# Kernel optimization log

Hardware: AMD Instinct MI355X
Metric: run time of the kernel (lower is better)

Reference implementation:

```python
import jax, jax.numpy as jnp
import numpy as np

BETA = 0.01  # soft-threshold level (init kwarg)
EPS = 1e-12


def vector_to_toeplitz(v):
    # v: [2N-1] complex generator; T[i, j] = v[N-1 + i - j], shape [N, N]
    n = (v.shape[0] + 1) // 2
    ii = jnp.arange(n)[:, None]
    jj = jnp.arange(n)[None, :]
    return v[(n - 1) + ii - jj]


def soft_thresh(z, beta):
    # complex soft-threshold (proximal op of beta*||.||_1):
    # z * max(|z| - beta, 0) / |z|
    mag = jnp.abs(z)
    scale = jnp.maximum(mag - beta, 0.0) / jnp.maximum(mag, EPS)
    return z * scale.astype(z.real.dtype)


def setup_inputs() -> dict:
    key = jax.random.key(0)
    ks = jax.random.split(key, 8)
    N, M, B = 1024, 256, 1024
    d = jnp.float32
    return {
        "v_re": jax.random.normal(ks[0], (2 * N - 1,), d),
        "v_im": jax.random.normal(ks[1], (2 * N - 1,), d),
        "W2_re": jax.random.normal(ks[2], (N, M), d) / np.sqrt(M),
        "W2_im": jax.random.normal(ks[3], (N, M), d) / np.sqrt(M),
        "x_re": jax.random.normal(ks[4], (N, B), d),
        "x_im": jax.random.normal(ks[5], (N, B), d),
        "y_re": jax.random.normal(ks[6], (M, B), d),
        "y_im": jax.random.normal(ks[7], (M, B), d),
    }


def reference(v_re, v_im, W2_re, W2_im, x_re, x_im, y_re, y_im):
    v = jax.lax.complex(v_re, v_im)      # [2N-1]
    W2 = jax.lax.complex(W2_re, W2_im)   # [N, M] (= A^H)
    x = jax.lax.complex(x_re, x_im)      # [N, B]
    y = jax.lax.complex(y_re, y_im)      # [M, B]
    W1 = vector_to_toeplitz(v)           # [N, N] Toeplitz
    # tpm(W1, x) + W2 @ y, then complex soft-threshold
    z = soft_thresh(W1 @ x + W2 @ y, BETA)  # [N, B]
    return z
```

## Files before the change

kernel.cpp:

```cpp
#include <hip/hip_runtime.h>
#include <hip/hip_fp16.h>
#include <cstdint>
#include <cstddef>


#define K_DIM 2560
#define BETA_F 0.01f
#define EPS_F  1e-12f

typedef __attribute__((ext_vector_type(8))) _Float16 half8;
typedef __attribute__((ext_vector_type(4))) _Float16 half4;
typedef __attribute__((ext_vector_type(4))) float   floatx4;

__device__ alignas(16) _Float16 g_Ap[1024 * K_DIM];
__device__ alignas(16) _Float16 g_Bt[2048 * K_DIM];

__global__ __launch_bounds__(256) void build_all(
    const float* __restrict__ v_re, const float* __restrict__ v_im,
    const float* __restrict__ W2_re, const float* __restrict__ W2_im,
    const float* __restrict__ x_re, const float* __restrict__ x_im,
    const float* __restrict__ y_re, const float* __restrict__ y_im)
{
    const int bx = blockIdx.x;
    if (bx < 1280) {
        int t = bx * 256 + threadIdx.x;
        int i  = t / 320;
        int c  = t - i * 320;
        int kp = c * 8;
        half8 h;
        if (kp < 1024) {
#pragma unroll
            for (int j = 0; j < 8; ++j) h[j] = (_Float16)v_re[1023 + i - kp - j];
        } else if (kp < 1280) {
            const float* s = W2_re + i * 256 + (kp - 1024);
#pragma unroll
            for (int j = 0; j < 8; ++j) h[j] = (_Float16)s[j];
        } else if (kp < 2304) {
            int k2 = kp - 1280;
#pragma unroll
            for (int j = 0; j < 8; ++j) h[j] = (_Float16)v_im[1023 + i - k2 - j];
        } else {
            const float* s = W2_im + i * 256 + (kp - 2304);
#pragma unroll
            for (int j = 0; j < 8; ++j) h[j] = (_Float16)s[j];
        }
        *reinterpret_cast<half8*>(g_Ap + (size_t)i * K_DIM + kp) = h;
        return;
    }
    __shared__ float lre[32][33];
    __shared__ float lim[32][33];
    int idx = bx - 1280;
    int bk  = idx % 40;
    int by  = idx / 40;
    const float* sre = (bk < 32) ? x_re : y_re;
    const float* sim = (bk < 32) ? x_im : y_im;
    int kb   = (bk < 32) ? bk : (bk - 32);
    int koff = (bk < 32) ? 0 : 1024;
    int k0 = kb * 32;
    int n0 = by * 32;
    int tid = threadIdx.x;
    int tx = tid & 31, ty = tid >> 5;
#pragma unroll
    for (int s = 0; s < 4; ++s) {
        int kk = ty + 8 * s;
        lre[kk][tx] = sre[(size_t)(k0 + kk) * 1024 + n0 + tx];
        lim[kk][tx] = sim[(size_t)(k0 + kk) * 1024 + n0 + tx];
    }
    __syncthreads();
    int lane_n = tid >> 3;
    int kq     = (tid & 7) * 4;
    half4 hre, him, hmim;
#pragma unroll
    for (int j = 0; j < 4; ++j) {
        float re = lre[kq + j][lane_n];
        float im = lim[kq + j][lane_n];
        hre[j]  = (_Float16)re;
        him[j]  = (_Float16)im;
        hmim[j] = (_Float16)(-im);
    }
    int n = n0 + lane_n;
    size_t kk2 = (size_t)koff + k0 + kq;
    _Float16* r0 = g_Bt + (size_t)(2 * n)     * K_DIM;
    _Float16* r1 = g_Bt + (size_t)(2 * n + 1) * K_DIM;
    *reinterpret_cast<half4*>(r0 + kk2)        = hre;
    *reinterpret_cast<half4*>(r0 + kk2 + 1280) = hmim;
    *reinterpret_cast<half4*>(r1 + kk2)        = him;
    *reinterpret_cast<half4*>(r1 + kk2 + 1280) = hre;
}

__global__ __launch_bounds__(256, 4) void gemm_fused(float* __restrict__ out,
                                                     int out_n)
{
    __shared__ __align__(16) _Float16 As[2 * 2 * 64 * 32];
    __shared__ __align__(16) _Float16 Bs[2 * 2 * 64 * 32];

    const int tid  = threadIdx.x;
    const int lane = tid & 63;
    const int w    = tid >> 6;
    const int wm   = w >> 1;
    const int wn   = w & 1;

    const int bid = blockIdx.x;
    const int xcd = bid & 7;
    const int t   = bid >> 3;
    const int mi0 = ((xcd & 1) * 8 + (t & 7)) * 64;
    const int ni0 = ((xcd >> 1) * 8 + (t >> 3)) * 64;

    floatx4 acc[2][2];
#pragma unroll
    for (int a = 0; a < 2; ++a)
#pragma unroll
        for (int b = 0; b < 2; ++b) acc[a][b] = (floatx4)0.0f;

    const int rS = tid >> 2;
    const int jS = tid & 3;
    const int s0 = ((rS & 15) >> 1) & 3;
    char* asW = (char*)As + rS * 64 + ((jS ^ s0) * 16);
    char* bsW = (char*)Bs + rS * 64 + ((jS ^ s0) * 16);
    const _Float16* gA = g_Ap + (size_t)(mi0 + rS) * K_DIM + jS * 8;
    const _Float16* gB = g_Bt + (size_t)(ni0 + rS) * K_DIM + jS * 8;

    const int rowA = lane & 15;
    const int q    = lane >> 4;
    const int coff = (q ^ ((rowA >> 1) & 3)) * 16;

    const int NIT = K_DIM / 64;

    half8 sA0[2], sA1[2], sB0[2], sB1[2];

    {
        half8 a0 = *reinterpret_cast<const half8*>(gA);
        half8 a1 = *reinterpret_cast<const half8*>(gA + 32);
        half8 b0 = *reinterpret_cast<const half8*>(gB);
        half8 b1 = *reinterpret_cast<const half8*>(gB + 32);
        sA0[1] = *reinterpret_cast<const half8*>(gA + 64);
        sA1[1] = *reinterpret_cast<const half8*>(gA + 96);
        sB0[1] = *reinterpret_cast<const half8*>(gB + 64);
        sB1[1] = *reinterpret_cast<const half8*>(gB + 96);
        *reinterpret_cast<half8*>(asW)        = a0;
        *reinterpret_cast<half8*>(asW + 4096) = a1;
        *reinterpret_cast<half8*>(bsW)        = b0;
        *reinterpret_cast<half8*>(bsW + 4096) = b1;
    }
    __syncthreads();

#pragma unroll 2
    for (int kt = 0; kt < NIT; ++kt) {
        const int cur = kt & 1;
        const int nxt = cur ^ 1;
        if (kt + 2 < NIT) {
            const _Float16* ga = gA + (size_t)(kt + 2) * 64;
            const _Float16* gb = gB + (size_t)(kt + 2) * 64;
            sA0[cur] = *reinterpret_cast<const half8*>(ga);
            sA1[cur] = *reinterpret_cast<const half8*>(ga + 32);
            sB0[cur] = *reinterpret_cast<const half8*>(gb);
            sB1[cur] = *reinterpret_cast<const half8*>(gb + 32);
        }
        const char* Ab = (const char*)As + cur * 8192;
        const char* Bb = (const char*)Bs + cur * 8192;
        half8 af[2][2], bf[2][2];
#pragma unroll
        for (int mi = 0; mi < 2; ++mi) {
            int r = wm * 32 + mi * 16 + rowA;
            af[mi][0] = *reinterpret_cast<const half8*>(Ab + r * 64 + coff);
            af[mi][1] = *reinterpret_cast<const half8*>(Ab + 4096 + r * 64 + coff);
        }
#pragma unroll
        for (int ni = 0; ni < 2; ++ni) {
            int r = wn * 32 + ni * 16 + rowA;
            bf[ni][0] = *reinterpret_cast<const half8*>(Bb + r * 64 + coff);
            bf[ni][1] = *reinterpret_cast<const half8*>(Bb + 4096 + r * 64 + coff);
        }
#pragma unroll
        for (int mi = 0; mi < 2; ++mi)
#pragma unroll
            for (int ni = 0; ni < 2; ++ni) {
                acc[mi][ni] = __builtin_amdgcn_mfma_f32_16x16x32_f16(
                    af[mi][0], bf[ni][0], acc[mi][ni], 0, 0, 0);
                acc[mi][ni] = __builtin_amdgcn_mfma_f32_16x16x32_f16(
                    af[mi][1], bf[ni][1], acc[mi][ni], 0, 0, 0);
            }
        if (kt + 1 < NIT) {
            char* aw = asW + nxt * 8192;
            char* bw = bsW + nxt * 8192;
            *reinterpret_cast<half8*>(aw)        = sA0[nxt];
            *reinterpret_cast<half8*>(aw + 4096) = sA1[nxt];
            *reinterpret_cast<half8*>(bw)        = sB0[nxt];
            *reinterpret_cast<half8*>(bw + 4096) = sB1[nxt];
        }
        __syncthreads();
    }

    const int colL  = lane & 15;
    const int rquad = (lane >> 4) * 4;
#pragma unroll
    for (int mi = 0; mi < 2; ++mi)
#pragma unroll
        for (int ni = 0; ni < 2; ++ni)
#pragma unroll
            for (int r = 0; r < 4; ++r) {
                float c = acc[mi][ni][r];
                float p = __shfl_xor(c, 1, 64);
                float mag = sqrtf(c * c + p * p);
                float s = fmaxf(mag - BETA_F, 0.0f) / fmaxf(mag, EPS_F);
                int row = mi0 + wm * 32 + mi * 16 + rquad + r;
                int col = ni0 + wn * 32 + ni * 16 + colL;
                if ((col & 1) == 0) {
                    size_t idx = (size_t)row * 1024 + (col >> 1);
                    if (idx < (size_t)out_n) out[idx] = c * s;
                }
            }
}

extern "C" void kernel_launch(void* const* d_in, const int* in_sizes, int n_in,
                              void* d_out, int out_size, void* d_ws, size_t ws_size,
                              hipStream_t stream) {
    (void)d_ws; (void)ws_size; (void)in_sizes; (void)n_in;
    const float* v_re  = (const float*)d_in[0];
    const float* v_im  = (const float*)d_in[1];
    const float* W2_re = (const float*)d_in[2];
    const float* W2_im = (const float*)d_in[3];
    const float* x_re  = (const float*)d_in[4];
    const float* x_im  = (const float*)d_in[5];
    const float* y_re  = (const float*)d_in[6];
    const float* y_im  = (const float*)d_in[7];
    float* out = (float*)d_out;

    build_all<<<2560, 256, 0, stream>>>(v_re, v_im, W2_re, W2_im,
                                        x_re, x_im, y_re, y_im);
    gemm_fused<<<512, 256, 0, stream>>>(out, out_size);
}
```

Before: 111.1 us.

## Stream GEMM tiles directly into LDS with global_load_lds

Replaces the register-staged global→LDS copy (load to registers, later write to LDS) with direct global_load_lds DMA-style loads into the next LDS buffer. Prefetch distance drops from two stages to one, and the swizzle moves from the LDS address to the global chunk index so LDS placement stays linear per wave. This aims to cut VGPR pressure and VALU/LDS-write instructions. In exchange, less latency is hidden, and the code relies on the barrier (and the compiler's vmcnt waits) for completion of async LDS writes.

```diff
diff --git a/kernel.cpp b/kernel.cpp
--- a/kernel.cpp
+++ b/kernel.cpp
@@ -88,6 +88,12 @@
     *reinterpret_cast<half4*>(r1 + kk2 + 1280) = hre;
 }
 
+__device__ __forceinline__ void load_lds16(const void* g, void* l) {
+    __builtin_amdgcn_global_load_lds(
+        (const __attribute__((address_space(1))) void*)g,
+        (__attribute__((address_space(3))) void*)l, 16, 0, 0);
+}
+
 __global__ __launch_bounds__(256, 4) void gemm_fused(float* __restrict__ out,
                                                      int out_n)
 {
@@ -112,13 +118,12 @@
 #pragma unroll
         for (int b = 0; b < 2; ++b) acc[a][b] = (floatx4)0.0f;
 
-    const int rS = tid >> 2;
-    const int jS = tid & 3;
-    const int s0 = ((rS & 15) >> 1) & 3;
-    char* asW = (char*)As + rS * 64 + ((jS ^ s0) * 16);
-    char* bsW = (char*)Bs + rS * 64 + ((jS ^ s0) * 16);
-    const _Float16* gA = g_Ap + (size_t)(mi0 + rS) * K_DIM + jS * 8;
-    const _Float16* gB = g_Bt + (size_t)(ni0 + rS) * K_DIM + jS * 8;
+    const int rowS  = (w * 16) + (lane >> 2);
+    const int chunk = (lane & 3) ^ ((lane >> 3) & 3);
+    const _Float16* gAl = g_Ap + (size_t)(mi0 + rowS) * K_DIM + chunk * 8;
+    const _Float16* gBl = g_Bt + (size_t)(ni0 + rowS) * K_DIM + chunk * 8;
+    char* asBase = (char*)As + w * 1024;
+    char* bsBase = (char*)Bs + w * 1024;
 
     const int rowA = lane & 15;
     const int q    = lane >> 4;
@@ -126,35 +131,24 @@
 
     const int NIT = K_DIM / 64;
 
-    half8 sA0[2], sA1[2], sB0[2], sB1[2];
-
-    {
-        half8 a0 = *reinterpret_cast<const half8*>(gA);
-        half8 a1 = *reinterpret_cast<const half8*>(gA + 32);
-        half8 b0 = *reinterpret_cast<const half8*>(gB);
-        half8 b1 = *reinterpret_cast<const half8*>(gB + 32);
-        sA0[1] = *reinterpret_cast<const half8*>(gA + 64);
-        sA1[1] = *reinterpret_cast<const half8*>(gA + 96);
-        sB0[1] = *reinterpret_cast<const half8*>(gB + 64);
-        sB1[1] = *reinterpret_cast<const half8*>(gB + 96);
-        *reinterpret_cast<half8*>(asW)        = a0;
-        *reinterpret_cast<half8*>(asW + 4096) = a1;
-        *reinterpret_cast<half8*>(bsW)        = b0;
-        *reinterpret_cast<half8*>(bsW + 4096) = b1;
+#pragma unroll
+    for (int ks = 0; ks < 2; ++ks) {
+        load_lds16(gAl + ks * 32, asBase + ks * 4096);
+        load_lds16(gBl + ks * 32, bsBase + ks * 4096);
     }
     __syncthreads();
 
-#pragma unroll 2
     for (int kt = 0; kt < NIT; ++kt) {
         const int cur = kt & 1;
         const int nxt = cur ^ 1;
-        if (kt + 2 < NIT) {
-            const _Float16* ga = gA + (size_t)(kt + 2) * 64;
-            const _Float16* gb = gB + (size_t)(kt + 2) * 64;
-            sA0[cur] = *reinterpret_cast<const half8*>(ga);
-            sA1[cur] = *reinterpret_cast<const half8*>(ga + 32);
-            sB0[cur] = *reinterpret_cast<const half8*>(gb);
-            sB1[cur] = *reinterpret_cast<const half8*>(gb + 32);
+        if (kt + 1 < NIT) {
+            const _Float16* ga = gAl + (size_t)(kt + 1) * 64;
+            const _Float16* gb = gBl + (size_t)(kt + 1) * 64;
+#pragma unroll
+            for (int ks = 0; ks < 2; ++ks) {
+                load_lds16(ga + ks * 32, asBase + nxt * 8192 + ks * 4096);
+                load_lds16(gb + ks * 32, bsBase + nxt * 8192 + ks * 4096);
+            }
         }
         const char* Ab = (const char*)As + cur * 8192;
         const char* Bb = (const char*)Bs + cur * 8192;
@@ -180,14 +174,6 @@
                 acc[mi][ni] = __builtin_amdgcn_mfma_f32_16x16x32_f16(
                     af[mi][1], bf[ni][1], acc[mi][ni], 0, 0, 0);
             }
-        if (kt + 1 < NIT) {
-            char* aw = asW + nxt * 8192;
-            char* bw = bsW + nxt * 8192;
-            *reinterpret_cast<half8*>(aw)        = sA0[nxt];
-            *reinterpret_cast<half8*>(aw + 4096) = sA1[nxt];
-            *reinterpret_cast<half8*>(bw)        = sB0[nxt];
-            *reinterpret_cast<half8*>(bw + 4096) = sB1[nxt];
-        }
         __syncthreads();
     }
 
```

Measured after the change: 115.8 us. 4.3% more time.
